# Kernel tuning notes

Measured on AMD Instinct MI355X. Metric: run time of the kernel, lower is better.

## Reference

```python
import jax, jax.numpy as jnp
import numpy as np

N, E = 50000, 800000
IN_DIM, HID, HEADS, OUT_DIM = 128, 64, 4, 40
NEG_SLOPE = 0.2


def setup_inputs() -> dict:
    key = jax.random.key(0)
    ks = jax.random.split(key, 12)
    x = jax.random.normal(ks[0], (N, IN_DIM), dtype=jnp.float32)
    edge_index = jax.random.randint(ks[1], (2, E), 0, N, dtype=jnp.int64)
    timesteps = jax.random.randint(ks[2], (N,), 0, 100, dtype=jnp.int64)
    s = 1.0 / np.sqrt(IN_DIM)
    W_proj = jax.random.uniform(ks[3], (IN_DIM, HID), jnp.float32, -s, s)
    b_proj = jnp.zeros((HID,), jnp.float32)
    time_emb = jax.random.normal(ks[4], (100, HID), dtype=jnp.float32)
    sg = 1.0 / np.sqrt(HID)
    W_gat = jax.random.uniform(ks[5], (HID, HEADS * HID), jnp.float32, -sg, sg)
    att_src = jax.random.uniform(ks[6], (HEADS, HID), jnp.float32, -sg, sg)
    att_dst = jax.random.uniform(ks[7], (HEADS, HID), jnp.float32, -sg, sg)
    b_gat = jnp.zeros((HEADS * HID,), jnp.float32)
    sc = 1.0 / np.sqrt(HEADS * HID)
    W_cls = jax.random.uniform(ks[8], (HEADS * HID, OUT_DIM), jnp.float32, -sc, sc)
    b_cls = jnp.zeros((OUT_DIM,), jnp.float32)
    return {"x": x, "edge_index": edge_index, "timesteps": timesteps,
            "W_proj": W_proj, "b_proj": b_proj, "time_emb": time_emb,
            "W_gat": W_gat, "att_src": att_src, "att_dst": att_dst, "b_gat": b_gat,
            "W_cls": W_cls, "b_cls": b_cls}


def reference(x, edge_index, timesteps, W_proj, b_proj, time_emb,
              W_gat, att_src, att_dst, b_gat, W_cls, b_cls):
    n = x.shape[0]
    # feature projection + ReLU + time embedding
    h0 = jax.nn.relu(x @ W_proj + b_proj) + time_emb[timesteps]  # [N, HID]
    # --- GATConv (PyG semantics, add_self_loops=True, concat heads) ---
    h = (h0 @ W_gat).reshape(n, HEADS, HID)              # [N, H, C]
    a_src = jnp.einsum('nhc,hc->nh', h, att_src)         # [N, H]
    a_dst = jnp.einsum('nhc,hc->nh', h, att_dst)
    loops = jnp.arange(n, dtype=edge_index.dtype)
    src = jnp.concatenate([edge_index[0], loops])        # [E+N]
    dst = jnp.concatenate([edge_index[1], loops])
    e = jax.nn.leaky_relu(a_src[src] + a_dst[dst], NEG_SLOPE)  # [E+N, H]
    # segment softmax over incoming edges per destination node
    m = jax.ops.segment_max(e, dst, num_segments=n)      # [N, H]
    p = jnp.exp(e - m[dst])
    denom = jax.ops.segment_sum(p, dst, num_segments=n)  # [N, H]
    alpha = p / (denom[dst] + 1e-16)                     # [E+N, H]
    msg = alpha[:, :, None] * h[src]                     # [E+N, H, C]
    agg = jax.ops.segment_sum(msg, dst, num_segments=n)  # [N, H, C]
    gat_out = agg.reshape(n, HEADS * HID) + b_gat
    # ReLU + (dropout is identity in eval) + classifier
    return jax.nn.relu(gat_out) @ W_cls + b_cls          # [N, OUT_DIM]
```

## Files before the change

kernel.cpp:

```cpp
#include <hip/hip_runtime.h>
#include <hip/hip_fp16.h>

#define IN_DIM 128
#define HID 64
#define HEADS 4
#define OUT_DIM 40
#define CAP 64
#define NEG 0.2f
#define PA_EPB 4096
#define BKT_SH 9
#define BKT_CAP 10240
#define GPAD 264
#define HGP 72

__device__ __forceinline__ float lrelu(float v) { return v > 0.f ? v : NEG * v; }

union HU { float2 f2; __half2 h2[2]; };
union HU2 { float4 f4; __half2 h2[4]; };

typedef _Float16 f16x8 __attribute__((ext_vector_type(8)));
typedef float f32x4 __attribute__((ext_vector_type(4)));
union FU { float4 f4; f16x8 v; };

__global__ __launch_bounds__(256) void partA_kernel(
    const int* __restrict__ ei, int E, int nbkt, int paBlocks,
    int* __restrict__ cnt, unsigned int* __restrict__ ebuf,
    const float* __restrict__ Wg, const float* __restrict__ attS,
    const float* __restrict__ attD, const float* __restrict__ Wc,
    const float* __restrict__ Wp,
    float* __restrict__ aSf, float* __restrict__ aDf,
    __half* __restrict__ WgT, __half* __restrict__ WcTg,
    __half* __restrict__ WpT, __half* __restrict__ BsdT)
{
    if (blockIdx.x >= paBlocks) {
        int gid = (blockIdx.x - paBlocks) * 256 + threadIdx.x;
        if (gid < 256) {
            int k = gid >> 2, hd = gid & 3;
            const float* wr = Wg + k * 256 + hd * 64;
            const float* as = attS + hd * 64;
            const float* ad = attD + hd * 64;
            float ss = 0.f, dd = 0.f;
            for (int c = 0; c < 64; ++c) { float w = wr[c]; ss += w * as[c]; dd += w * ad[c]; }
            aSf[k * 4 + hd] = ss;
            aDf[k * 4 + hd] = dd;
        } else if (gid < 256 + 256 * HID) {
            int i = gid - 256;
            int o = i >> 6, k = i & 63;
            WgT[i] = __float2half(Wg[k * 256 + o]);
        } else if (gid < 256 + 256 * HID + OUT_DIM * 256) {
            int i = gid - 256 - 256 * HID;
            int o = i >> 8, k = i & 255;
            WcTg[i] = __float2half(Wc[k * OUT_DIM + o]);
        } else if (gid < 26880 + HID * IN_DIM) {
            int i = gid - 26880;
            int o = i >> 7, k = i & 127;
            WpT[i] = __float2half(Wp[k * HID + o]);
        } else if (gid < 26880 + HID * IN_DIM + 16 * HID) {
            int i = gid - 26880 - HID * IN_DIM;
            int n2 = i >> 6, k = i & 63;
            float v = 0.f;
            if (n2 < 8) {
                int hd = n2 & 3;
                const float* wr = Wg + k * 256 + hd * 64;
                const float* av = (n2 < 4) ? (attS + hd * 64) : (attD + hd * 64);
                for (int c = 0; c < 64; ++c) v += wr[c] * av[c];
            }
            BsdT[i] = __float2half(v);
        }
        return;
    }

    __shared__ int localCnt[128];
    __shared__ int baseArr[128];
    for (int i = threadIdx.x; i < nbkt; i += 256) localCnt[i] = 0;
    __syncthreads();

    const int e0 = blockIdx.x * PA_EPB + threadIdx.x;
    unsigned short l[16];
#pragma unroll
    for (int j = 0; j < 16; ++j) {
        int e = e0 + j * 256;
        if (e < E) {
            int d = ei[E + e];
            l[j] = (unsigned short)atomicAdd(&localCnt[d >> BKT_SH], 1);
        }
    }
    __syncthreads();
    for (int i = threadIdx.x; i < nbkt; i += 256)
        baseArr[i] = atomicAdd(&cnt[i], localCnt[i]);
    __syncthreads();
#pragma unroll
    for (int j = 0; j < 16; ++j) {
        int e = e0 + j * 256;
        if (e < E) {
            int s = ei[e];
            int d = ei[E + e];
            int b = d >> BKT_SH;
            int off = baseArr[b] + (int)l[j];
            if (off < BKT_CAP)
                ebuf[(size_t)b * BKT_CAP + off] =
                    ((unsigned)(d & ((1 << BKT_SH) - 1)) << 16) | (unsigned)s;
        }
    }
}

__global__ __launch_bounds__(256) void partBproj_kernel(
    const unsigned int* __restrict__ ebuf, const int* __restrict__ cnt,
    int* __restrict__ deg, unsigned short* __restrict__ csr, int nbkt,
    const float* __restrict__ x, const __half* __restrict__ WpT,
    const float* __restrict__ bp, const float* __restrict__ temb,
    const int* __restrict__ ts, const __half* __restrict__ BsdT,
    __half* __restrict__ h0h, float* __restrict__ aS, float* __restrict__ aD, int N)
{
    __shared__ __align__(16) char smem[32 * HGP * 2];

    if ((int)blockIdx.x < nbkt) {
        int* cntL = (int*)smem;
        const int b = blockIdx.x;
        for (int i = threadIdx.x; i < 512; i += 256) cntL[i] = 0;
        __syncthreads();

        int cb = cnt[b]; cb = cb < BKT_CAP ? cb : BKT_CAP;
        const unsigned int* eb = ebuf + (size_t)b * BKT_CAP;
        const int d0 = b << BKT_SH;
        for (int i = threadIdx.x; i < cb; i += 256) {
            unsigned v = eb[i];
            int dloc = v >> 16;
            int slot = atomicAdd(&cntL[dloc], 1);
            if (slot < CAP)
                csr[((size_t)(d0 + dloc) << 6) + slot] = (unsigned short)(v & 0xFFFFu);
        }
        __syncthreads();
        for (int i = threadIdx.x; i < 512; i += 256) {
            int d = d0 + i;
            if (d < N) deg[d] = cntL[i];
        }
        return;
    }

    __half* h0L = (__half*)smem;
    const int t = threadIdx.x;
    const int lane = t & 63, wq = t >> 6;
    const int m16 = lane & 15, quad = lane >> 4;
    const int mt = wq >> 1;
    const int ntb = (wq & 1) * 2;
    const int nodeBase = ((int)blockIdx.x - nbkt) * 32;

    f32x4 acc[2];
    acc[0] = (f32x4){0.f, 0.f, 0.f, 0.f};
    acc[1] = (f32x4){0.f, 0.f, 0.f, 0.f};

    {
        int n = nodeBase + mt * 16 + m16; n = n < N ? n : N - 1;
        const float* xr = x + (size_t)n * IN_DIM;
#pragma unroll
        for (int ks = 0; ks < 4; ++ks) {
            float4 xa = *(const float4*)(xr + ks * 32 + quad * 8);
            float4 xb = *(const float4*)(xr + ks * 32 + quad * 8 + 4);
            HU2 u;
            u.h2[0] = __floats2half2_rn(xa.x, xa.y);
            u.h2[1] = __floats2half2_rn(xa.z, xa.w);
            u.h2[2] = __floats2half2_rn(xb.x, xb.y);
            u.h2[3] = __floats2half2_rn(xb.z, xb.w);
            FU a; a.f4 = u.f4;
#pragma unroll
            for (int q = 0; q < 2; ++q) {
                int o = (ntb + q) * 16 + m16;
                FU b; b.f4 = *(const float4*)(WpT + o * IN_DIM + ks * 32 + quad * 8);
                acc[q] = __builtin_amdgcn_mfma_f32_16x16x32_f16(a.v, b.v, acc[q], 0, 0, 0);
            }
        }
    }

    {
        float bv[2];
#pragma unroll
        for (int q = 0; q < 2; ++q) bv[q] = bp[(ntb + q) * 16 + m16];
#pragma unroll
        for (int r = 0; r < 4; ++r) {
            int nloc = mt * 16 + quad * 4 + r;
            int n = nodeBase + nloc;
            if (n < N) {
                int tv = ts[n];
                const float* te = temb + (size_t)tv * HID;
#pragma unroll
                for (int q = 0; q < 2; ++q) {
                    int c = (ntb + q) * 16 + m16;
                    float v = fmaxf(acc[q][r] + bv[q], 0.f) + te[c];
                    h0L[nloc * HGP + c] = __float2half(v);
                }
            }
        }
    }
    __syncthreads();

    {
        int row = t >> 3, ch = (t & 7) * 8;
        int n = nodeBase + row;
        if (n < N)
            *(float4*)(h0h + (size_t)n * HID + ch) = *(const float4*)(h0L + row * HGP + ch);
    }

    if (wq < 2) {
        f32x4 acc2 = (f32x4){0.f, 0.f, 0.f, 0.f};
#pragma unroll
        for (int ks = 0; ks < 2; ++ks) {
            FU a; a.f4 = *(const float4*)(h0L + (wq * 16 + m16) * HGP + ks * 32 + quad * 8);
            FU b; b.f4 = *(const float4*)(BsdT + m16 * 64 + ks * 32 + quad * 8);
            acc2 = __builtin_amdgcn_mfma_f32_16x16x32_f16(a.v, b.v, acc2, 0, 0, 0);
        }
#pragma unroll
        for (int r = 0; r < 4; ++r) {
            int n = nodeBase + wq * 16 + quad * 4 + r;
            if (n < N) {
                if (m16 < 4)      aS[n * 4 + m16]       = acc2[r];
                else if (m16 < 8) aD[n * 4 + (m16 - 4)] = acc2[r];
            }
        }
    }
}

__global__ __launch_bounds__(256) void agg_kernel(
    const __half* __restrict__ h0h, const float* __restrict__ aS,
    const float* __restrict__ aD, const int* __restrict__ deg,
    const unsigned short* __restrict__ csr, __half* __restrict__ agg0h, int N)
{
    __shared__ float p_lds[4 * CAP * HEADS];
    __shared__ int   s_lds[4 * CAP];

    const int t = threadIdx.x;
    const int lane = t & 63, wq = t >> 6;
    const int n = blockIdx.x * 4 + wq;
    if (n >= N) return;
    const int hd16 = lane >> 4, li = lane & 15;

    const float adn = aD[n * 4 + hd16];
    const float es = lrelu(aS[n * 4 + hd16] + adn);

    int dn = deg[n]; dn = dn < CAP ? dn : CAP;
    const unsigned short* cs = csr + (size_t)n * CAP;
    float* pL = p_lds + wq * CAP * HEADS;
    int*   sL = s_lds + wq * CAP;

    float m = -1e30f;
    for (int i = li; i < dn; i += 16) {
        int src = cs[i];
        if (hd16 == 0) sL[i] = src << 7;
        float e = lrelu(aS[src * 4 + hd16] + adn);
        pL[i * HEADS + hd16] = e;
        m = fmaxf(m, e);
    }
#pragma unroll
    for (int off = 8; off > 0; off >>= 1)
        m = fmaxf(m, __shfl_xor(m, off));
    m = fmaxf(m, es);
    float mh[4], esh[4];
#pragma unroll
    for (int h = 0; h < 4; ++h) {
        mh[h]  = __shfl(m, h * 16);
        esh[h] = __shfl(es, h * 16);
    }

    float sp = 0.f;
    for (int idx = lane; idx < dn * 4; idx += 64) {
        float p = __expf(pL[idx] - mh[idx & 3]);
        pL[idx] = p;
        sp += p;
    }
#pragma unroll
    for (int off = 4; off < 64; off <<= 1)
        sp += __shfl_xor(sp, off);
    float pselfh[4], invh[4];
#pragma unroll
    for (int h = 0; h < 4; ++h) {
        float sh = __shfl(sp, h);
        pselfh[h] = __expf(esh[h] - mh[h]);
        invh[h] = 1.f / (sh + pselfh[h] + 1e-16f);
    }

    const int half = lane >> 5;
    const int ch2 = lane & 31;
    const char* hb = (const char*)h0h;
    const int laneByte = ch2 << 2;

    float2 acc[4];
    {
        float lo = 0.f, hi = 0.f;
        if (half == 0) {
            __half2 v2 = *(const __half2*)(hb + ((size_t)n << 7) + laneByte);
            float2 f = __half22float2(v2);
            lo = f.x; hi = f.y;
        }
#pragma unroll
        for (int h = 0; h < 4; ++h) {
            acc[h].x = pselfh[h] * lo;
            acc[h].y = pselfh[h] * hi;
        }
    }
    int i = 0;
    for (; i + 8 <= dn; i += 8) {
        int off0 = sL[i + 0 + half];
        int off1 = sL[i + 2 + half];
        int off2 = sL[i + 4 + half];
        int off3 = sL[i + 6 + half];
        __half2 v0 = *(const __half2*)(hb + off0 + laneByte);
        __half2 v1 = *(const __half2*)(hb + off1 + laneByte);
        __half2 v2 = *(const __half2*)(hb + off2 + laneByte);
        __half2 v3 = *(const __half2*)(hb + off3 + laneByte);
        float4 p0 = *(const float4*)(pL + (i + 0 + half) * 4);
        float4 p1 = *(const float4*)(pL + (i + 2 + half) * 4);
        float4 p2 = *(const float4*)(pL + (i + 4 + half) * 4);
        float4 p3 = *(const float4*)(pL + (i + 6 + half) * 4);
        float2 f;
        f = __half22float2(v0);
        acc[0].x += p0.x * f.x; acc[0].y += p0.x * f.y;
        acc[1].x += p0.y * f.x; acc[1].y += p0.y * f.y;
        acc[2].x += p0.z * f.x; acc[2].y += p0.z * f.y;
        acc[3].x += p0.w * f.x; acc[3].y += p0.w * f.y;
        f = __half22float2(v1);
        acc[0].x += p1.x * f.x; acc[0].y += p1.x * f.y;
        acc[1].x += p1.y * f.x; acc[1].y += p1.y * f.y;
        acc[2].x += p1.z * f.x; acc[2].y += p1.z * f.y;
        acc[3].x += p1.w * f.x; acc[3].y += p1.w * f.y;
        f = __half22float2(v2);
        acc[0].x += p2.x * f.x; acc[0].y += p2.x * f.y;
        acc[1].x += p2.y * f.x; acc[1].y += p2.y * f.y;
        acc[2].x += p2.z * f.x; acc[2].y += p2.z * f.y;
        acc[3].x += p2.w * f.x; acc[3].y += p2.w * f.y;
        f = __half22float2(v3);
        acc[0].x += p3.x * f.x; acc[0].y += p3.x * f.y;
        acc[1].x += p3.y * f.x; acc[1].y += p3.y * f.y;
        acc[2].x += p3.z * f.x; acc[2].y += p3.z * f.y;
        acc[3].x += p3.w * f.x; acc[3].y += p3.w * f.y;
    }
    for (; i + 2 <= dn; i += 2) {
        int off0 = sL[i + half];
        __half2 v0 = *(const __half2*)(hb + off0 + laneByte);
        float4 p0 = *(const float4*)(pL + (i + half) * 4);
        float2 f = __half22float2(v0);
        acc[0].x += p0.x * f.x; acc[0].y += p0.x * f.y;
        acc[1].x += p0.y * f.x; acc[1].y += p0.y * f.y;
        acc[2].x += p0.z * f.x; acc[2].y += p0.z * f.y;
        acc[3].x += p0.w * f.x; acc[3].y += p0.w * f.y;
    }
    if (i < dn && half == 0) {
        int off0 = sL[i];
        __half2 v0 = *(const __half2*)(hb + off0 + laneByte);
        float4 p0 = *(const float4*)(pL + i * 4);
        float2 f = __half22float2(v0);
        acc[0].x += p0.x * f.x; acc[0].y += p0.x * f.y;
        acc[1].x += p0.y * f.x; acc[1].y += p0.y * f.y;
        acc[2].x += p0.z * f.x; acc[2].y += p0.z * f.y;
        acc[3].x += p0.w * f.x; acc[3].y += p0.w * f.y;
    }
#pragma unroll
    for (int h = 0; h < 4; ++h) {
        acc[h].x += __shfl_xor(acc[h].x, 32);
        acc[h].y += __shfl_xor(acc[h].y, 32);
    }
    if (lane < 32) {
        __half2* dst = (__half2*)(agg0h + (size_t)n * 256);
#pragma unroll
        for (int h = 0; h < 4; ++h)
            dst[h * 32 + ch2] = __floats2half2_rn(acc[h].x * invh[h],
                                                  acc[h].y * invh[h]);
    }
}

__global__ __launch_bounds__(256) void gatcls_kernel(
    const __half* __restrict__ agg0h, const __half* __restrict__ WgT,
    const float* __restrict__ bg, const __half* __restrict__ WcTg,
    const float* __restrict__ bc, float* __restrict__ out, int N)
{
    __shared__ __half gtile[32 * GPAD];

    const int t = threadIdx.x;
    const int lane = t & 63, wq = t >> 6;
    const int m16 = lane & 15, quad = lane >> 4;
    const int nodeBase = blockIdx.x * 32;

    {
        const int h = wq;
        f32x4 acc[2][4];
#pragma unroll
        for (int mt = 0; mt < 2; ++mt)
#pragma unroll
            for (int nt = 0; nt < 4; ++nt)
                acc[mt][nt] = (f32x4){0.f, 0.f, 0.f, 0.f};

#pragma unroll
        for (int ks = 0; ks < 2; ++ks) {
            FU a[2], b[4];
#pragma unroll
            for (int mt = 0; mt < 2; ++mt) {
                int n = nodeBase + mt * 16 + m16; n = n < N ? n : N - 1;
                a[mt].f4 = *(const float4*)(agg0h + (size_t)n * 256 + h * 64 + ks * 32 + quad * 8);
            }
#pragma unroll
            for (int nt = 0; nt < 4; ++nt) {
                int o = h * 64 + nt * 16 + m16;
                b[nt].f4 = *(const float4*)(WgT + o * 64 + ks * 32 + quad * 8);
            }
#pragma unroll
            for (int mt = 0; mt < 2; ++mt)
#pragma unroll
                for (int nt = 0; nt < 4; ++nt)
                    acc[mt][nt] = __builtin_amdgcn_mfma_f32_16x16x32_f16(
                        a[mt].v, b[nt].v, acc[mt][nt], 0, 0, 0);
        }
#pragma unroll
        for (int nt = 0; nt < 4; ++nt) {
            int o = h * 64 + nt * 16 + m16;
            float bv = bg[o];
#pragma unroll
            for (int mt = 0; mt < 2; ++mt) {
#pragma unroll
                for (int r = 0; r < 4; ++r) {
                    int nloc = mt * 16 + quad * 4 + r;
                    gtile[nloc * GPAD + o] = __float2half(fmaxf(acc[mt][nt][r] + bv, 0.f));
                }
            }
        }
    }
    __syncthreads();

    {
        const int mt = wq >> 1;
        const int ntCount = (wq & 1) ? 1 : 2;
        const int ntBase = (wq & 1) ? 2 : 0;
        f32x4 acc2[2];
        acc2[0] = (f32x4){0.f, 0.f, 0.f, 0.f};
        acc2[1] = (f32x4){0.f, 0.f, 0.f, 0.f};
#pragma unroll
        for (int ks = 0; ks < 8; ++ks) {
            FU a; a.f4 = *(const float4*)(gtile + (mt * 16 + m16) * GPAD + ks * 32 + quad * 8);
            for (int q = 0; q < ntCount; ++q) {
                int o = (ntBase + q) * 16 + m16;
                int oc = o < OUT_DIM ? o : OUT_DIM - 1;
                FU b; b.f4 = *(const float4*)(WcTg + oc * 256 + ks * 32 + quad * 8);
                acc2[q] = __builtin_amdgcn_mfma_f32_16x16x32_f16(a.v, b.v, acc2[q], 0, 0, 0);
            }
        }
        for (int q = 0; q < ntCount; ++q) {
            int o = (ntBase + q) * 16 + m16;
            if (o < OUT_DIM) {
                float bv = bc[o];
#pragma unroll
                for (int r = 0; r < 4; ++r) {
                    int n = nodeBase + mt * 16 + quad * 4 + r;
                    if (n < N) out[(size_t)n * OUT_DIM + o] = acc2[q][r] + bv;
                }
            }
        }
    }
}

extern "C" void kernel_launch(void* const* d_in, const int* in_sizes, int n_in,
                              void* d_out, int out_size, void* d_ws, size_t ws_size,
                              hipStream_t stream) {
    const float* x    = (const float*)d_in[0];
    const int*   ei   = (const int*)d_in[1];
    const int*   ts   = (const int*)d_in[2];
    const float* Wp   = (const float*)d_in[3];
    const float* bp   = (const float*)d_in[4];
    const float* temb = (const float*)d_in[5];
    const float* Wg   = (const float*)d_in[6];
    const float* attS = (const float*)d_in[7];
    const float* attD = (const float*)d_in[8];
    const float* bg   = (const float*)d_in[9];
    const float* Wc   = (const float*)d_in[10];
    const float* bc   = (const float*)d_in[11];
    float* out = (float*)d_out;

    const int N = in_sizes[0] / IN_DIM;
    const int E = in_sizes[1] / 2;
    const int nbkt = (N + (1 << BKT_SH) - 1) >> BKT_SH;

    char* w = (char*)d_ws;
    __half*         h0h   = (__half*)w;         w += (size_t)N * HID * 2;
    __half*         agg0h = (__half*)w;         w += (size_t)N * 256 * 2;
    float*          aS    = (float*)w;          w += (size_t)N * HEADS * 4;
    float*          aD    = (float*)w;          w += (size_t)N * HEADS * 4;
    int*            deg   = (int*)w;            w += (size_t)N * 4;
    unsigned short* csr   = (unsigned short*)w; w += (size_t)N * CAP * 2;
    unsigned int*   ebuf  = (unsigned int*)w;   w += (size_t)nbkt * BKT_CAP * 4;
    int*            cnt   = (int*)w;            w += (size_t)nbkt * 4;
    float*          aSf   = (float*)w;          w += 256 * 4;
    float*          aDf   = (float*)w;          w += 256 * 4;
    __half*         WgT   = (__half*)w;         w += (size_t)256 * HID * 2;
    __half*         WcTg  = (__half*)w;         w += (size_t)OUT_DIM * 256 * 2;
    __half*         WpT   = (__half*)w;         w += (size_t)HID * IN_DIM * 2;
    __half*         BsdT  = (__half*)w;         w += (size_t)16 * HID * 2;

    const int paBlocks = (E + PA_EPB - 1) / PA_EPB;
    const int prepWork = 256 + 256 * HID + OUT_DIM * 256
                       + HID * IN_DIM + 16 * HID;
    const int prepBlocks = (prepWork + 255) / 256;
    const int projBlocks = (N + 31) / 32;

    hipMemsetAsync(cnt, 0, (size_t)nbkt * 4, stream);
    partA_kernel<<<paBlocks + prepBlocks, 256, 0, stream>>>(
        ei, E, nbkt, paBlocks, cnt, ebuf, Wg, attS, attD, Wc, Wp,
        aSf, aDf, WgT, WcTg, WpT, BsdT);
    partBproj_kernel<<<nbkt + projBlocks, 256, 0, stream>>>(
        ebuf, cnt, deg, csr, nbkt, x, WpT, bp, temb, ts, BsdT, h0h, aS, aD, N);
    agg_kernel<<<(N + 3) / 4, 256, 0, stream>>>(h0h, aS, aD, deg, csr, agg0h, N);
    gatcls_kernel<<<(N + 31) / 32, 256, 0, stream>>>(agg0h, WgT, bg, WcTg, bc, out, N);
}
```

Before: 198.6 us.

## Restructure launch schedule: fuse edge binning with projection, split CSR build

Weight transposes and the bucket-counter reset move into a small prep kernel, which replaces the memset and drops the unused aSf/aDf computation. Edge binning now shares a launch with the feature projection, since both only need the prep outputs. The per-bucket CSR build becomes its own kernel. The schedule is meant to overlap binning with the projection GEMM and drop one API call, at the cost of one extra kernel launch.

Result: no change. 199.4 us (+0.4%).

```diff
diff --git a/kernel.cpp b/kernel.cpp
--- a/kernel.cpp
+++ b/kernel.cpp
@@ -22,91 +22,46 @@
 typedef float f32x4 __attribute__((ext_vector_type(4)));
 union FU { float4 f4; f16x8 v; };
 
-__global__ __launch_bounds__(256) void partA_kernel(
-    const int* __restrict__ ei, int E, int nbkt, int paBlocks,
-    int* __restrict__ cnt, unsigned int* __restrict__ ebuf,
+__global__ __launch_bounds__(256) void prep_kernel(
     const float* __restrict__ Wg, const float* __restrict__ attS,
     const float* __restrict__ attD, const float* __restrict__ Wc,
     const float* __restrict__ Wp,
-    float* __restrict__ aSf, float* __restrict__ aDf,
     __half* __restrict__ WgT, __half* __restrict__ WcTg,
-    __half* __restrict__ WpT, __half* __restrict__ BsdT)
+    __half* __restrict__ WpT, __half* __restrict__ BsdT,
+    int* __restrict__ cnt, int nbkt)
 {
-    if (blockIdx.x >= paBlocks) {
-        int gid = (blockIdx.x - paBlocks) * 256 + threadIdx.x;
-        if (gid < 256) {
-            int k = gid >> 2, hd = gid & 3;
+    int gid = blockIdx.x * 256 + threadIdx.x;
+    if (gid < 16384) {
+        int o = gid >> 6, k = gid & 63;
+        WgT[gid] = __float2half(Wg[k * 256 + o]);
+    } else if (gid < 26624) {
+        int i = gid - 16384;
+        int o = i >> 8, k = i & 255;
+        WcTg[i] = __float2half(Wc[k * OUT_DIM + o]);
+    } else if (gid < 34816) {
+        int i = gid - 26624;
+        int o = i >> 7, k = i & 127;
+        WpT[i] = __float2half(Wp[k * HID + o]);
+    } else if (gid < 35840) {
+        int i = gid - 34816;
+        int n2 = i >> 6, k = i & 63;
+        float v = 0.f;
+        if (n2 < 8) {
+            int hd = n2 & 3;
             const float* wr = Wg + k * 256 + hd * 64;
-            const float* as = attS + hd * 64;
-            const float* ad = attD + hd * 64;
-            float ss = 0.f, dd = 0.f;
-            for (int c = 0; c < 64; ++c) { float w = wr[c]; ss += w * as[c]; dd += w * ad[c]; }
-            aSf[k * 4 + hd] = ss;
-            aDf[k * 4 + hd] = dd;
-        } else if (gid < 256 + 256 * HID) {
-            int i = gid - 256;
-            int o = i >> 6, k = i & 63;
-            WgT[i] = __float2half(Wg[k * 256 + o]);
-        } else if (gid < 256 + 256 * HID + OUT_DIM * 256) {
-            int i = gid - 256 - 256 * HID;
-            int o = i >> 8, k = i & 255;
-            WcTg[i] = __float2half(Wc[k * OUT_DIM + o]);
-        } else if (gid < 26880 + HID * IN_DIM) {
-            int i = gid - 26880;
-            int o = i >> 7, k = i & 127;
-            WpT[i] = __float2half(Wp[k * HID + o]);
-        } else if (gid < 26880 + HID * IN_DIM + 16 * HID) {
-            int i = gid - 26880 - HID * IN_DIM;
-            int n2 = i >> 6, k = i & 63;
-            float v = 0.f;
-            if (n2 < 8) {
-                int hd = n2 & 3;
-                const float* wr = Wg + k * 256 + hd * 64;
-                const float* av = (n2 < 4) ? (attS + hd * 64) : (attD + hd * 64);
-                for (int c = 0; c < 64; ++c) v += wr[c] * av[c];
-            }
-            BsdT[i] = __float2half(v);
-        }
-        return;
-    }
-
-    __shared__ int localCnt[128];
-    __shared__ int baseArr[128];
-    for (int i = threadIdx.x; i < nbkt; i += 256) localCnt[i] = 0;
-    __syncthreads();
-
-    const int e0 = blockIdx.x * PA_EPB + threadIdx.x;
-    unsigned short l[16];
-#pragma unroll
-    for (int j = 0; j < 16; ++j) {
-        int e = e0 + j * 256;
-        if (e < E) {
-            int d = ei[E + e];
-            l[j] = (unsigned short)atomicAdd(&localCnt[d >> BKT_SH], 1);
-        }
-    }
-    __syncthreads();
-    for (int i = threadIdx.x; i < nbkt; i += 256)
-        baseArr[i] = atomicAdd(&cnt[i], localCnt[i]);
-    __syncthreads();
-#pragma unroll
-    for (int j = 0; j < 16; ++j) {
-        int e = e0 + j * 256;
-        if (e < E) {
-            int s = ei[e];
-            int d = ei[E + e];
-            int b = d >> BKT_SH;
-            int off = baseArr[b] + (int)l[j];
-            if (off < BKT_CAP)
-                ebuf[(size_t)b * BKT_CAP + off] =
-                    ((unsigned)(d & ((1 << BKT_SH) - 1)) << 16) | (unsigned)s;
-        }
-    }
-}
-
-__global__ __launch_bounds__(256) void partBproj_kernel(
-    const unsigned int* __restrict__ ebuf, const int* __restrict__ cnt,
-    int* __restrict__ deg, unsigned short* __restrict__ csr, int nbkt,
+            const float* av = (n2 < 4) ? (attS + hd * 64) : (attD + hd * 64);
+            for (int c = 0; c < 64; ++c) v += wr[c] * av[c];
+        }
+        BsdT[i] = __float2half(v);
+    } else {
+        int i = gid - 35840;
+        if (i < nbkt) cnt[i] = 0;
+    }
+}
+
+__global__ __launch_bounds__(256) void binproj_kernel(
+    const int* __restrict__ ei, int E, int nbkt, int nbin,
+    int* __restrict__ cnt, unsigned int* __restrict__ ebuf,
     const float* __restrict__ x, const __half* __restrict__ WpT,
     const float* __restrict__ bp, const float* __restrict__ temb,
     const int* __restrict__ ts, const __half* __restrict__ BsdT,
@@ -114,26 +69,38 @@
 {
     __shared__ __align__(16) char smem[32 * HGP * 2];
 
-    if ((int)blockIdx.x < nbkt) {
-        int* cntL = (int*)smem;
-        const int b = blockIdx.x;
-        for (int i = threadIdx.x; i < 512; i += 256) cntL[i] = 0;
+    if ((int)blockIdx.x < nbin) {
+        int* localCnt = (int*)smem;
+        int* baseArr  = (int*)smem + 128;
+        for (int i = threadIdx.x; i < nbkt; i += 256) localCnt[i] = 0;
         __syncthreads();
 
-        int cb = cnt[b]; cb = cb < BKT_CAP ? cb : BKT_CAP;
-        const unsigned int* eb = ebuf + (size_t)b * BKT_CAP;
-        const int d0 = b << BKT_SH;
-        for (int i = threadIdx.x; i < cb; i += 256) {
-            unsigned v = eb[i];
-            int dloc = v >> 16;
-            int slot = atomicAdd(&cntL[dloc], 1);
-            if (slot < CAP)
-                csr[((size_t)(d0 + dloc) << 6) + slot] = (unsigned short)(v & 0xFFFFu);
+        const int e0 = blockIdx.x * PA_EPB + threadIdx.x;
+        unsigned short l[16];
+#pragma unroll
+        for (int j = 0; j < 16; ++j) {
+            int e = e0 + j * 256;
+            if (e < E) {
+                int d = ei[E + e];
+                l[j] = (unsigned short)atomicAdd(&localCnt[d >> BKT_SH], 1);
+            }
         }
         __syncthreads();
-        for (int i = threadIdx.x; i < 512; i += 256) {
-            int d = d0 + i;
-            if (d < N) deg[d] = cntL[i];
+        for (int i = threadIdx.x; i < nbkt; i += 256)
+            baseArr[i] = atomicAdd(&cnt[i], localCnt[i]);
+        __syncthreads();
+#pragma unroll
+        for (int j = 0; j < 16; ++j) {
+            int e = e0 + j * 256;
+            if (e < E) {
+                int s = ei[e];
+                int d = ei[E + e];
+                int b = d >> BKT_SH;
+                int off = baseArr[b] + (int)l[j];
+                if (off < BKT_CAP)
+                    ebuf[(size_t)b * BKT_CAP + off] =
+                        ((unsigned)(d & ((1 << BKT_SH) - 1)) << 16) | (unsigned)s;
+            }
         }
         return;
     }
@@ -144,7 +111,7 @@
     const int m16 = lane & 15, quad = lane >> 4;
     const int mt = wq >> 1;
     const int ntb = (wq & 1) * 2;
-    const int nodeBase = ((int)blockIdx.x - nbkt) * 32;
+    const int nodeBase = ((int)blockIdx.x - nbin) * 32;
 
     f32x4 acc[2];
     acc[0] = (f32x4){0.f, 0.f, 0.f, 0.f};
@@ -217,6 +184,32 @@
                 else if (m16 < 8) aD[n * 4 + (m16 - 4)] = acc2[r];
             }
         }
+    }
+}
+
+__global__ __launch_bounds__(256) void partB_kernel(
+    const unsigned int* __restrict__ ebuf, const int* __restrict__ cnt,
+    int* __restrict__ deg, unsigned short* __restrict__ csr, int N)
+{
+    __shared__ int cntL[512];
+    const int b = blockIdx.x;
+    for (int i = threadIdx.x; i < 512; i += 256) cntL[i] = 0;
+    __syncthreads();
+
+    int cb = cnt[b]; cb = cb < BKT_CAP ? cb : BKT_CAP;
+    const unsigned int* eb = ebuf + (size_t)b * BKT_CAP;
+    const int d0 = b << BKT_SH;
+    for (int i = threadIdx.x; i < cb; i += 256) {
+        unsigned v = eb[i];
+        int dloc = v >> 16;
+        int slot = atomicAdd(&cntL[dloc], 1);
+        if (slot < CAP)
+            csr[((size_t)(d0 + dloc) << 6) + slot] = (unsigned short)(v & 0xFFFFu);
+    }
+    __syncthreads();
+    for (int i = threadIdx.x; i < 512; i += 256) {
+        int d = d0 + i;
+        if (d < N) deg[d] = cntL[i];
     }
 }
 
@@ -485,25 +478,21 @@
     unsigned short* csr   = (unsigned short*)w; w += (size_t)N * CAP * 2;
     unsigned int*   ebuf  = (unsigned int*)w;   w += (size_t)nbkt * BKT_CAP * 4;
     int*            cnt   = (int*)w;            w += (size_t)nbkt * 4;
-    float*          aSf   = (float*)w;          w += 256 * 4;
-    float*          aDf   = (float*)w;          w += 256 * 4;
     __half*         WgT   = (__half*)w;         w += (size_t)256 * HID * 2;
     __half*         WcTg  = (__half*)w;         w += (size_t)OUT_DIM * 256 * 2;
     __half*         WpT   = (__half*)w;         w += (size_t)HID * IN_DIM * 2;
     __half*         BsdT  = (__half*)w;         w += (size_t)16 * HID * 2;
 
-    const int paBlocks = (E + PA_EPB - 1) / PA_EPB;
-    const int prepWork = 256 + 256 * HID + OUT_DIM * 256
-                       + HID * IN_DIM + 16 * HID;
+    const int nbin       = (E + PA_EPB - 1) / PA_EPB;
+    const int prepWork   = 35840 + nbkt;
     const int prepBlocks = (prepWork + 255) / 256;
     const int projBlocks = (N + 31) / 32;
 
-    hipMemsetAsync(cnt, 0, (size_t)nbkt * 4, stream);
-    partA_kernel<<<paBlocks + prepBlocks, 256, 0, stream>>>(
-        ei, E, nbkt, paBlocks, cnt, ebuf, Wg, attS, attD, Wc, Wp,
-        aSf, aDf, WgT, WcTg, WpT, BsdT);
-    partBproj_kernel<<<nbkt + projBlocks, 256, 0, stream>>>(
-        ebuf, cnt, deg, csr, nbkt, x, WpT, bp, temb, ts, BsdT, h0h, aS, aD, N);
+    prep_kernel<<<prepBlocks, 256, 0, stream>>>(
+        Wg, attS, attD, Wc, Wp, WgT, WcTg, WpT, BsdT, cnt, nbkt);
+    binproj_kernel<<<nbin + projBlocks, 256, 0, stream>>>(
+        ei, E, nbkt, nbin, cnt, ebuf, x, WpT, bp, temb, ts, BsdT, h0h, aS, aD, N);
+    partB_kernel<<<nbkt, 256, 0, stream>>>(ebuf, cnt, deg, csr, N);
     agg_kernel<<<(N + 3) / 4, 256, 0, stream>>>(h0h, aS, aD, deg, csr, agg0h, N);
     gatcls_kernel<<<(N + 31) / 32, 256, 0, stream>>>(agg0h, WgT, bg, WcTg, bc, out, N);
 }
```
